# Kernel tuning notes

Measured on AMD Instinct MI355X. Metric: run time of the kernel, lower is better.

## Reference

```python
import jax, jax.numpy as jnp
import numpy as np

B, F, D, H = 16384, 39, 16, 2   # batch, fields, embed_dim, heads
VOCAB = 10000                    # per-field vocab
DH = D * H                       # attention output dim per layer (no head split)


def setup_inputs() -> dict:
    key = jax.random.key(0)
    ks = jax.random.split(key, 32)
    def n(k, shape, s=0.05):
        return jax.random.normal(k, shape, jnp.float32) * s
    inp = {"x": jax.random.randint(ks[0], (B, F), 0, VOCAB, dtype=jnp.int32)}
    inp["emb"] = n(ks[1], (F * VOCAB, D))
    idx = 2
    for i, din in enumerate([D, DH, DH]):  # layer0: 16->32, layers 1-2: 32->32
        for nm in ["wq", "wk", "wv", "wr"]:
            inp[f"{nm}{i}"] = n(ks[idx], (din, DH)); idx += 1
    prev = F * DH  # 1248 after flatten
    for i, u in enumerate([128, 64, 32, 1], 1):
        inp[f"w{i}"] = n(ks[idx], (prev, u)); idx += 1
        inp[f"b{i}"] = jnp.zeros((u,), jnp.float32)
        prev = u
    return inp


def reference(x, emb,
              wq0, wk0, wv0, wr0,
              wq1, wk1, wv1, wr1,
              wq2, wk2, wv2, wr2,
              w1, b1, w2, b2, w3, b3, w4, b4):
    offsets = jnp.arange(F, dtype=jnp.int32) * VOCAB
    e = emb[x + offsets]                                   # [B, F, D]
    for wq, wk, wv, wr in [(wq0, wk0, wv0, wr0),
                           (wq1, wk1, wv1, wr1),
                           (wq2, wk2, wv2, wr2)]:
        q = jnp.einsum('bfd,de->bfe', e, wq)               # [B, F, DH]
        k = jnp.einsum('bfd,de->bfe', e, wk)
        v = jnp.einsum('bfd,de->bfe', e, wv)
        att = jax.nn.softmax(jnp.einsum('bfe,bge->bfg', q, k), axis=-1)  # [B,F,F], no scaling
        out = jnp.einsum('bfg,bge->bfe', att, v) + jnp.einsum('bfd,de->bfe', e, wr)
        e = jax.nn.relu(out)
    h = e.reshape(B, F * DH)
    for w, b in [(w1, b1), (w2, b2), (w3, b3)]:
        h = jax.nn.relu(h @ w + b)
    return jax.nn.sigmoid(h @ w4 + b4)                     # [B, 1]
```

## Files before the change

### kernel.cpp

```cpp
#include <hip/hip_runtime.h>
#include <math.h>

#define NF   39
#define NB   16384
#define NVOC 10000

typedef unsigned short u16;
typedef unsigned int   u32;
typedef float f32x4 __attribute__((ext_vector_type(4)));
typedef float f32x2 __attribute__((ext_vector_type(2)));
typedef short s16x8 __attribute__((ext_vector_type(8)));
typedef unsigned int u32x2 __attribute__((ext_vector_type(2)));

#define E3_U16   20447232u
#define WOFF_W1  9216u
#define NSWZ     179200

__device__ __forceinline__ u32 bfadj(float x){
    u32 u = __float_as_uint(x);
    return u + 0x7fffu + ((u >> 16) & 1u);
}
__device__ __forceinline__ u32 pk2(float a, float b){
#if __has_builtin(__builtin_amdgcn_cvt_pk_bf16_f32)
    auto t = __builtin_amdgcn_cvt_pk_bf16_f32(a, b);
    u32 r; __builtin_memcpy(&r, &t, 4); return r;
#else
    return __builtin_amdgcn_perm(bfadj(a), bfadj(b), 0x03020706u);
#endif
}
__device__ __forceinline__ u16 f2bf(float f){ return (u16)(bfadj(f) >> 16); }

__device__ __forceinline__ float fexp2(float x){
#if __has_builtin(__builtin_amdgcn_exp2f)
    return __builtin_amdgcn_exp2f(x);
#else
    return exp2f(x);
#endif
}
__device__ __forceinline__ float frcp(float x){
#if __has_builtin(__builtin_amdgcn_rcpf)
    return __builtin_amdgcn_rcpf(x);
#else
    return 1.f / x;
#endif
}

__device__ __forceinline__ void wave_sync(){
    asm volatile("s_waitcnt lgkmcnt(0)" ::: "memory");
}
__device__ __forceinline__ f32x4 mfma16(s16x8 a, s16x8 b, f32x4 c){
    return __builtin_amdgcn_mfma_f32_16x16x32_bf16(a, b, c, 0, 0, 0);
}
__device__ __forceinline__ void store4(u16* p, f32x4 v){
    *(uint2*)p = make_uint2(pk2(v[0], v[1]), pk2(v[2], v[3]));
}

__device__ __forceinline__ f32x2 pkadd(f32x2 a, f32x2 b){
    f32x2 d; asm("v_pk_add_f32 %0, %1, %2" : "=v"(d) : "v"(a), "v"(b)); return d;
}
__device__ __forceinline__ f32x2 pkmul(f32x2 a, f32x2 b){
    f32x2 d; asm("v_pk_mul_f32 %0, %1, %2" : "=v"(d) : "v"(a), "v"(b)); return d;
}

__device__ __forceinline__ void swap32(u32 &a, u32 &b){
    asm("v_permlane32_swap_b32 %0, %1" : "+v"(a), "+v"(b));
}
__device__ __forceinline__ void swap16(u32 &a, u32 &b){
    asm("v_permlane16_swap_b32 %0, %1" : "+v"(a), "+v"(b));
}
__device__ __forceinline__ s16x8 fragPack(u32 a0, u32 a1, u32 b0, u32 b1){
    swap32(a0, b0); swap16(a0, b0);
    swap32(a1, b1); swap16(a1, b1);
    union { u32 w[4]; s16x8 v; } u;
    u.w[0] = a0; u.w[1] = a1; u.w[2] = b0; u.w[3] = b1;
    return u.v;
}
__device__ __forceinline__ s16x8 fragCC(f32x4 A, f32x4 B){
    return fragPack(pk2(A[0],A[1]), pk2(A[2],A[3]), pk2(B[0],B[1]), pk2(B[2],B[3]));
}
__device__ __forceinline__ s16x8 fragC0(f32x4 A){
    return fragPack(pk2(A[0],A[1]), pk2(A[2],A[3]), 0u, 0u);
}
__device__ __forceinline__ s16x8 fragCCn(f32x4 A, f32x4 B, f32x2 iv){
    f32x2 a01 = pkmul(__builtin_shufflevector(A, A, 0, 1), iv);
    f32x2 a23 = pkmul(__builtin_shufflevector(A, A, 2, 3), iv);
    f32x2 b01 = pkmul(__builtin_shufflevector(B, B, 0, 1), iv);
    f32x2 b23 = pkmul(__builtin_shufflevector(B, B, 2, 3), iv);
    return fragPack(pk2(a01.x,a01.y), pk2(a23.x,a23.y),
                    pk2(b01.x,b01.y), pk2(b23.x,b23.y));
}
__device__ __forceinline__ s16x8 fragC0n(f32x4 A, f32x2 iv){
    f32x2 a01 = pkmul(__builtin_shufflevector(A, A, 0, 1), iv);
    f32x2 a23 = pkmul(__builtin_shufflevector(A, A, 2, 3), iv);
    return fragPack(pk2(a01.x,a01.y), pk2(a23.x,a23.y), 0u, 0u);
}
__device__ __forceinline__ float xadd16(float t){
    u32 a = __float_as_uint(t), b = a;
    swap16(a, b);
    return __uint_as_float(a) + __uint_as_float(b);
}
__device__ __forceinline__ float xadd32(float t){
    u32 a = __float_as_uint(t), b = a;
    swap32(a, b);
    return __uint_as_float(a) + __uint_as_float(b);
}

__global__ void __launch_bounds__(256) swz_kernel(
    const float* __restrict__ wq0, const float* __restrict__ wk0,
    const float* __restrict__ wv0, const float* __restrict__ wr0,
    const float* __restrict__ wq1, const float* __restrict__ wk1,
    const float* __restrict__ wv1, const float* __restrict__ wr1,
    const float* __restrict__ wq2, const float* __restrict__ wk2,
    const float* __restrict__ wv2, const float* __restrict__ wr2,
    const float* __restrict__ w1, const float* __restrict__ w2,
    const float* __restrict__ w3, u16* __restrict__ ws)
{
    int gid = (int)blockIdx.x*256 + (int)threadIdx.x;
    if (gid >= NSWZ) return;
    int w    = gid & 511;
    int lane = w >> 3, j = w & 7;
    int n    = lane & 15, quad = lane >> 4;
    int kin  = quad*8 + j;
    float val;
    if (gid < 9216){
        int l = gid / 3072;
        int rr = gid - l*3072;
        int kind = rr >> 10;
        int a    = (rr >> 9) & 1;
        int din  = l ? 32 : 16;
        const float *WQ, *WK, *WV, *WR;
        if (l == 0){ WQ=wq0; WK=wk0; WV=wv0; WR=wr0; }
        else if (l == 1){ WQ=wq1; WK=wk1; WV=wv1; WR=wr1; }
        else { WQ=wq2; WK=wk2; WV=wv2; WR=wr2; }
        if (kind == 0){
            int dp = a*16 + n;
            float s = 0.f;
            if (dp < din && kin < din){
                float acc = 0.f;
                for (int e = 0; e < 32; ++e)
                    acc += WQ[kin*32 + e] * WK[dp*32 + e];
                s = acc * 1.44269504f;
            }
            val = s;
        } else {
            const float* W = (kind == 1) ? WV : WR;
            val = (kin < din) ? W[kin*32 + a*16 + n] : 0.f;
        }
    } else if (gid < 9216 + 159744){
        int tt = (gid - 9216) >> 9;
        int ks = tt >> 3, nt = tt & 7;
        val = w1[(ks*32 + kin)*128 + nt*16 + n];
    } else if (gid < 9216 + 159744 + 8192){
        int tt = (gid - (9216+159744)) >> 9;
        int ks = tt >> 2, nt = tt & 3;
        val = w2[(ks*32 + kin)*64 + nt*16 + n];
    } else {
        int tt = (gid - (9216+159744+8192)) >> 9;
        int ks = tt >> 1, nt = tt & 1;
        val = w3[(ks*32 + kin)*32 + nt*16 + n];
    }
    ws[E3_U16 + gid] = f2bf(val);
}

__global__ void __launch_bounds__(256, 4) attn_kernel(
    const int* __restrict__ x, const float* __restrict__ emb,
    u16* __restrict__ ws)
{
    __shared__ __align__(16) u16 lds[4*1536];
    const int tid  = (int)threadIdx.x;
    const int wid  = tid >> 6, lane = tid & 63;
    const int h    = lane >> 4, nl = lane & 15;
    const int r    = (int)blockIdx.x*4 + wid;

    u16* eBuf = lds + wid*1536;
    const u16* wmat = ws + E3_U16;
    const f32x4 z = {0.f, 0.f, 0.f, 0.f};

    f32x4 ci;
#pragma unroll
    for (int reg = 0; reg < 4; ++reg)
        ci[reg] = (h*4 + reg >= 7) ? -1e30f : 0.f;

    if (lane < 48){
        int f = lane, mt = f >> 4, fl = f & 15;
        u16* row = eBuf + mt*512 + fl*8;
        if (f < NF){
            const float4* ep = (const float4*)(emb + ((size_t)(x[r*NF + f] + f*NVOC))*16);
            float4 e0 = ep[0], e1 = ep[1], e2 = ep[2], e3 = ep[3];
            *(uint4*)(row)       = make_uint4(pk2(e0.x,e0.y), pk2(e0.z,e0.w),
                                              pk2(e1.x,e1.y), pk2(e1.z,e1.w));
            *(uint4*)(row + 128) = make_uint4(pk2(e2.x,e2.y), pk2(e2.z,e2.w),
                                              pk2(e3.x,e3.y), pk2(e3.z,e3.w));
        } else {
            *(uint4*)(row)       = make_uint4(0,0,0,0);
            *(uint4*)(row + 128) = make_uint4(0,0,0,0);
        }
        *(uint4*)(row + 256) = make_uint4(0,0,0,0);
        *(uint4*)(row + 384) = make_uint4(0,0,0,0);
    }
    wave_sync();
    s16x8 bE[3];
#pragma unroll
    for (int nt = 0; nt < 3; ++nt)
        bE[nt] = *(const s16x8*)(eBuf + nt*512 + lane*8);

#pragma unroll 1
    for (int L = 0; L < 3; ++L){
        const u16* wL = wmat + L*3072;

        s16x8 bT[3];
        {
            s16x8 g0 = *(const s16x8*)(wL +       lane*8);
            s16x8 g1 = *(const s16x8*)(wL + 512 + lane*8);
#pragma unroll
            for (int nt = 0; nt < 3; ++nt)
                bT[nt] = fragCC(mfma16(g0, bE[nt], z), mfma16(g1, bE[nt], z));
        }
        s16x8 aV[2][2];
        {
            s16x8 v0 = *(const s16x8*)(wL + 1024 + lane*8);
            s16x8 v1 = *(const s16x8*)(wL + 1536 + lane*8);
#pragma unroll
            for (int emt = 0; emt < 2; ++emt){
                s16x8 vb = emt ? v1 : v0;
                f32x4 c0 = mfma16(bE[0], vb, z);
                f32x4 c1 = mfma16(bE[1], vb, z);
                f32x4 c2 = mfma16(bE[2], vb, z);
                aV[0][emt] = fragCC(c0, c1);
                aV[1][emt] = fragC0(c2);
            }
        }
        f32x4 S[3][3];
#pragma unroll
        for (int mtg = 0; mtg < 3; ++mtg)
#pragma unroll
        for (int nt = 0; nt < 3; ++nt)
            S[mtg][nt] = mfma16(bE[mtg], bT[nt], (mtg == 2) ? ci : z);

        float inv[3];
#pragma unroll
        for (int nt = 0; nt < 3; ++nt){
            f32x2 acc2 = {0.f, 0.f};
#pragma unroll
            for (int mtg = 0; mtg < 3; ++mtg){
#pragma unroll
                for (int reg = 0; reg < 4; ++reg)
                    S[mtg][nt][reg] = fexp2(S[mtg][nt][reg]);
                acc2 = pkadd(acc2, __builtin_shufflevector(S[mtg][nt], S[mtg][nt], 0, 1));
                acc2 = pkadd(acc2, __builtin_shufflevector(S[mtg][nt], S[mtg][nt], 2, 3));
            }
            inv[nt] = frcp(xadd32(xadd16(acc2.x + acc2.y)));
        }
        inv[2] = (nl < 7) ? inv[2] : 0.f;

        f32x4 R[2][3];
        {
            s16x8 r0 = *(const s16x8*)(wL + 2048 + lane*8);
            s16x8 r1 = *(const s16x8*)(wL + 2560 + lane*8);
#pragma unroll
            for (int nt = 0; nt < 3; ++nt){
                R[0][nt] = mfma16(r0, bE[nt], z);
                R[1][nt] = mfma16(r1, bE[nt], z);
            }
        }
        if (nl >= 7){ R[0][2] = z; R[1][2] = z; }

        if (L < 2){
#pragma unroll
            for (int nt = 0; nt < 3; ++nt){
                f32x2 iv = {inv[nt], inv[nt]};
                s16x8 p0 = fragCCn(S[0][nt], S[1][nt], iv);
                s16x8 p1 = fragC0n(S[2][nt], iv);
                f32x4 oc[2];
#pragma unroll
                for (int emt = 0; emt < 2; ++emt){
                    f32x4 o = mfma16(aV[1][emt], p1,
                              mfma16(aV[0][emt], p0, R[emt][nt]));
#pragma unroll
                    for (int reg = 0; reg < 4; ++reg)
                        o[reg] = fmaxf(o[reg], 0.f);
                    oc[emt] = o;
                }
                bE[nt] = fragCC(oc[0], oc[1]);
            }
        } else {
            int st = r >> 4, sm = r & 15;
            u32 base = (u32)(st*39)*512u + (u32)(sm*8 + (h>>1)*128 + (h&1)*4);
#pragma unroll
            for (int nt = 0; nt < 3; ++nt){
                f32x2 iv = {inv[nt], inv[nt]};
                s16x8 p0 = fragCCn(S[0][nt], S[1][nt], iv);
                s16x8 p1 = fragC0n(S[2][nt], iv);
                int f = nt*16 + nl;
#pragma unroll
                for (int emt = 0; emt < 2; ++emt){
                    f32x4 o = mfma16(aV[1][emt], p1,
                              mfma16(aV[0][emt], p0, R[emt][nt]));
#pragma unroll
                    for (int reg = 0; reg < 4; ++reg)
                        o[reg] = fmaxf(o[reg], 0.f);
                    if (f < NF){
                        u32x2 pkd = { pk2(o[0], o[1]), pk2(o[2], o[3]) };
                        __builtin_nontemporal_store(
                            pkd, (u32x2*)(ws + base + (u32)f*512u + emt*256));
                    }
                }
            }
        }
    }
}

__global__ void __launch_bounds__(256, 4) mlp_kernel(
    const float* __restrict__ b1, const float* __restrict__ b2,
    const float* __restrict__ b3, const float* __restrict__ w4,
    const float* __restrict__ b4, const u16* __restrict__ ws,
    float* __restrict__ out)
{
    __shared__ __align__(16) float red[8192];
    __shared__ __align__(16) u16 h1t[2048];
    __shared__ __align__(16) u16 h2t[1024];
    __shared__ float part[32];
    const int tid = (int)threadIdx.x;
    const int w   = tid >> 6, lane = tid & 63;
    const int h   = lane >> 4, nl = lane & 15;
    const int st  = (int)blockIdx.x;
    const int A_off = nl*8 + (h>>1)*128 + (h&1)*4;

    const u16* w1b = ws + E3_U16 + WOFF_W1;
    const u16* w2b = w1b + 159744u;
    const u16* w3b = w2b + 8192u;
    const f32x4 z = {0.f,0.f,0.f,0.f};

    f32x4 acc[8];
#pragma unroll
    for (int nt = 0; nt < 8; ++nt) acc[nt] = z;
#pragma unroll 2
    for (int ks = w; ks < 39; ks += 4){
        s16x8 aE = __builtin_nontemporal_load(
            (const s16x8*)(ws + (u32)(st*39 + ks)*512u + lane*8));
#pragma unroll
        for (int nt = 0; nt < 8; ++nt){
            s16x8 aW = *(const s16x8*)(w1b + (ks*8 + nt)*512 + lane*8);
            acc[nt] = mfma16(aW, aE, acc[nt]);
        }
    }
#pragma unroll
    for (int nt = 0; nt < 8; ++nt)
        *(f32x4*)(red + (w*8 + nt)*256 + lane*4) = acc[nt];
    __syncthreads();

#pragma unroll
    for (int t = 0; t < 2; ++t){
        int ft = 2*w + t;
        f32x4 s = *(const f32x4*)(red + (0*8 + ft)*256 + lane*4);
#pragma unroll
        for (int p = 1; p < 4; ++p){
            f32x4 q = *(const f32x4*)(red + (p*8 + ft)*256 + lane*4);
#pragma unroll
            for (int reg = 0; reg < 4; ++reg) s[reg] += q[reg];
        }
        float4 bv = *(const float4*)(b1 + ft*16 + h*4);
        f32x4 v;
        v[0] = fmaxf(s[0] + bv.x, 0.f);
        v[1] = fmaxf(s[1] + bv.y, 0.f);
        v[2] = fmaxf(s[2] + bv.z, 0.f);
        v[3] = fmaxf(s[3] + bv.w, 0.f);
        store4(h1t + ft*256 + A_off, v);
    }
    __syncthreads();

    {
        f32x4 a2 = z;
#pragma unroll
        for (int ks = 0; ks < 4; ++ks){
            s16x8 aW = *(const s16x8*)(w2b + (ks*4 + w)*512 + lane*8);
            s16x8 bH = *(const s16x8*)(h1t + ks*512 + lane*8);
            a2 = mfma16(aW, bH, a2);
        }
        float4 bv = *(const float4*)(b2 + w*16 + h*4);
        f32x4 v;
        v[0] = fmaxf(a2[0] + bv.x, 0.f);
        v[1] = fmaxf(a2[1] + bv.y, 0.f);
        v[2] = fmaxf(a2[2] + bv.z, 0.f);
        v[3] = fmaxf(a2[3] + bv.w, 0.f);
        store4(h2t + (w>>1)*512 + (w&1)*256 + A_off, v);
    }
    __syncthreads();

    if (w < 2){
        f32x4 a3 = z;
#pragma unroll
        for (int ks = 0; ks < 2; ++ks){
            s16x8 aW = *(const s16x8*)(w3b + (ks*2 + w)*512 + lane*8);
            s16x8 bH = *(const s16x8*)(h2t + ks*512 + lane*8);
            a3 = mfma16(aW, bH, a3);
        }
        float4 b3v = *(const float4*)(b3 + w*16 + h*4);
        float4 w4v = *(const float4*)(w4 + w*16 + h*4);
        float t = fmaxf(a3[0] + b3v.x, 0.f)*w4v.x
                + fmaxf(a3[1] + b3v.y, 0.f)*w4v.y
                + fmaxf(a3[2] + b3v.z, 0.f)*w4v.z
                + fmaxf(a3[3] + b3v.w, 0.f)*w4v.w;
        t += __shfl_xor(t, 16, 64);
        t += __shfl_xor(t, 32, 64);
        if (h == 0) part[w*16 + nl] = t;
    }
    __syncthreads();
    if (tid < 16){
        float zz = part[tid] + part[16 + tid] + b4[0];
        out[st*16 + tid] = 1.f/(1.f + __expf(-zz));
    }
}

extern "C" void kernel_launch(void* const* d_in, const int* in_sizes, int n_in,
                              void* d_out, int out_size, void* d_ws, size_t ws_size,
                              hipStream_t stream)
{
    (void)in_sizes; (void)n_in; (void)ws_size; (void)out_size;
    const int*   x   = (const int*)d_in[0];
    const float* emb = (const float*)d_in[1];
    u16* ws = (u16*)d_ws;

    swz_kernel<<<(NSWZ+255)/256, 256, 0, stream>>>(
        (const float*)d_in[2],  (const float*)d_in[3],  (const float*)d_in[4],  (const float*)d_in[5],
        (const float*)d_in[6],  (const float*)d_in[7],  (const float*)d_in[8],  (const float*)d_in[9],
        (const float*)d_in[10], (const float*)d_in[11], (const float*)d_in[12], (const float*)d_in[13],
        (const float*)d_in[14], (const float*)d_in[16], (const float*)d_in[18], ws);

    attn_kernel<<<NB/4, 256, 0, stream>>>(x, emb, ws);

    mlp_kernel<<<NB/16, 256, 0, stream>>>(
        (const float*)d_in[15], (const float*)d_in[17], (const float*)d_in[19],
        (const float*)d_in[20], (const float*)d_in[21], ws, (float*)d_out);
}
```

Baseline: 196.5 us.

## Give each wave its own MLP row tile and use cached attention stores

The MLP kernel is reorganised so each wave owns a full 16-row tile and runs all 39 K-steps of layer 1, plus layers 2-4, alone. This removes the 32 KB shared-memory reduction buffer and the block-wide barriers, using only wave-level syncs. The grid shrinks to a quarter, with four tiles per block. Separately, the attention kernel's output stores switch from nontemporal to ordinary stores, so the data the MLP kernel reads next may stay in cache. The cost is a longer serial K loop per wave and less latency hiding inside each tile.

```diff
diff --git a/kernel.cpp b/kernel.cpp
--- a/kernel.cpp
+++ b/kernel.cpp
@@ -299,11 +299,9 @@
 #pragma unroll
                     for (int reg = 0; reg < 4; ++reg)
                         o[reg] = fmaxf(o[reg], 0.f);
-                    if (f < NF){
-                        u32x2 pkd = { pk2(o[0], o[1]), pk2(o[2], o[3]) };
-                        __builtin_nontemporal_store(
-                            pkd, (u32x2*)(ws + base + (u32)f*512u + emt*256));
-                    }
+                    if (f < NF)
+                        *(uint2*)(ws + base + (u32)f*512u + emt*256) =
+                            make_uint2(pk2(o[0], o[1]), pk2(o[2], o[3]));
                 }
             }
         }
@@ -316,16 +314,16 @@
     const float* __restrict__ b4, const u16* __restrict__ ws,
     float* __restrict__ out)
 {
-    __shared__ __align__(16) float red[8192];
-    __shared__ __align__(16) u16 h1t[2048];
-    __shared__ __align__(16) u16 h2t[1024];
-    __shared__ float part[32];
+    __shared__ __align__(16) u16 h1t[4*2048];
+    __shared__ __align__(16) u16 h2t[4*1024];
     const int tid = (int)threadIdx.x;
     const int w   = tid >> 6, lane = tid & 63;
     const int h   = lane >> 4, nl = lane & 15;
-    const int st  = (int)blockIdx.x;
+    const int st  = (int)blockIdx.x*4 + w;
     const int A_off = nl*8 + (h>>1)*128 + (h&1)*4;
 
+    u16* h1w = h1t + w*2048;
+    u16* h2w = h2t + w*1024;
     const u16* w1b = ws + E3_U16 + WOFF_W1;
     const u16* w2b = w1b + 159744u;
     const u16* w3b = w2b + 8192u;
@@ -335,7 +333,7 @@
 #pragma unroll
     for (int nt = 0; nt < 8; ++nt) acc[nt] = z;
 #pragma unroll 2
-    for (int ks = w; ks < 39; ks += 4){
+    for (int ks = 0; ks < 39; ++ks){
         s16x8 aE = __builtin_nontemporal_load(
             (const s16x8*)(ws + (u32)(st*39 + ks)*512u + lane*8));
 #pragma unroll
@@ -345,70 +343,67 @@
         }
     }
 #pragma unroll
-    for (int nt = 0; nt < 8; ++nt)
-        *(f32x4*)(red + (w*8 + nt)*256 + lane*4) = acc[nt];
-    __syncthreads();
-
-#pragma unroll
-    for (int t = 0; t < 2; ++t){
-        int ft = 2*w + t;
-        f32x4 s = *(const f32x4*)(red + (0*8 + ft)*256 + lane*4);
-#pragma unroll
-        for (int p = 1; p < 4; ++p){
-            f32x4 q = *(const f32x4*)(red + (p*8 + ft)*256 + lane*4);
-#pragma unroll
-            for (int reg = 0; reg < 4; ++reg) s[reg] += q[reg];
-        }
-        float4 bv = *(const float4*)(b1 + ft*16 + h*4);
+    for (int nt = 0; nt < 8; ++nt){
+        float4 bv = *(const float4*)(b1 + nt*16 + h*4);
         f32x4 v;
-        v[0] = fmaxf(s[0] + bv.x, 0.f);
-        v[1] = fmaxf(s[1] + bv.y, 0.f);
-        v[2] = fmaxf(s[2] + bv.z, 0.f);
-        v[3] = fmaxf(s[3] + bv.w, 0.f);
-        store4(h1t + ft*256 + A_off, v);
-    }
-    __syncthreads();
+        v[0] = fmaxf(acc[nt][0] + bv.x, 0.f);
+        v[1] = fmaxf(acc[nt][1] + bv.y, 0.f);
+        v[2] = fmaxf(acc[nt][2] + bv.z, 0.f);
+        v[3] = fmaxf(acc[nt][3] + bv.w, 0.f);
+        store4(h1w + nt*256 + A_off, v);
+    }
+    wave_sync();
 
     {
-        f32x4 a2 = z;
+        f32x4 a2[4];
+#pragma unroll
+        for (int nt = 0; nt < 4; ++nt) a2[nt] = z;
 #pragma unroll
         for (int ks = 0; ks < 4; ++ks){
-            s16x8 aW = *(const s16x8*)(w2b + (ks*4 + w)*512 + lane*8);
-            s16x8 bH = *(const s16x8*)(h1t + ks*512 + lane*8);
-            a2 = mfma16(aW, bH, a2);
-        }
-        float4 bv = *(const float4*)(b2 + w*16 + h*4);
-        f32x4 v;
-        v[0] = fmaxf(a2[0] + bv.x, 0.f);
-        v[1] = fmaxf(a2[1] + bv.y, 0.f);
-        v[2] = fmaxf(a2[2] + bv.z, 0.f);
-        v[3] = fmaxf(a2[3] + bv.w, 0.f);
-        store4(h2t + (w>>1)*512 + (w&1)*256 + A_off, v);
-    }
-    __syncthreads();
-
-    if (w < 2){
-        f32x4 a3 = z;
-#pragma unroll
-        for (int ks = 0; ks < 2; ++ks){
-            s16x8 aW = *(const s16x8*)(w3b + (ks*2 + w)*512 + lane*8);
-            s16x8 bH = *(const s16x8*)(h2t + ks*512 + lane*8);
-            a3 = mfma16(aW, bH, a3);
-        }
-        float4 b3v = *(const float4*)(b3 + w*16 + h*4);
-        float4 w4v = *(const float4*)(w4 + w*16 + h*4);
-        float t = fmaxf(a3[0] + b3v.x, 0.f)*w4v.x
-                + fmaxf(a3[1] + b3v.y, 0.f)*w4v.y
-                + fmaxf(a3[2] + b3v.z, 0.f)*w4v.z
-                + fmaxf(a3[3] + b3v.w, 0.f)*w4v.w;
+            s16x8 bH = *(const s16x8*)(h1w + ks*512 + lane*8);
+#pragma unroll
+            for (int nt = 0; nt < 4; ++nt){
+                s16x8 aW = *(const s16x8*)(w2b + (ks*4 + nt)*512 + lane*8);
+                a2[nt] = mfma16(aW, bH, a2[nt]);
+            }
+        }
+#pragma unroll
+        for (int nt = 0; nt < 4; ++nt){
+            float4 bv = *(const float4*)(b2 + nt*16 + h*4);
+            f32x4 v;
+            v[0] = fmaxf(a2[nt][0] + bv.x, 0.f);
+            v[1] = fmaxf(a2[nt][1] + bv.y, 0.f);
+            v[2] = fmaxf(a2[nt][2] + bv.z, 0.f);
+            v[3] = fmaxf(a2[nt][3] + bv.w, 0.f);
+            store4(h2w + (nt>>1)*512 + (nt&1)*256 + A_off, v);
+        }
+    }
+    wave_sync();
+
+    {
+        float t = 0.f;
+#pragma unroll
+        for (int nt = 0; nt < 2; ++nt){
+            f32x4 a3 = z;
+#pragma unroll
+            for (int ks = 0; ks < 2; ++ks){
+                s16x8 aW = *(const s16x8*)(w3b + (ks*2 + nt)*512 + lane*8);
+                s16x8 bH = *(const s16x8*)(h2w + ks*512 + lane*8);
+                a3 = mfma16(aW, bH, a3);
+            }
+            float4 b3v = *(const float4*)(b3 + nt*16 + h*4);
+            float4 w4v = *(const float4*)(w4 + nt*16 + h*4);
+            t += fmaxf(a3[0] + b3v.x, 0.f)*w4v.x
+               + fmaxf(a3[1] + b3v.y, 0.f)*w4v.y
+               + fmaxf(a3[2] + b3v.z, 0.f)*w4v.z
+               + fmaxf(a3[3] + b3v.w, 0.f)*w4v.w;
+        }
         t += __shfl_xor(t, 16, 64);
         t += __shfl_xor(t, 32, 64);
-        if (h == 0) part[w*16 + nl] = t;
-    }
-    __syncthreads();
-    if (tid < 16){
-        float zz = part[tid] + part[16 + tid] + b4[0];
-        out[st*16 + tid] = 1.f/(1.f + __expf(-zz));
+        if (h == 0){
+            float zz = t + b4[0];
+            out[st*16 + nl] = 1.f/(1.f + __expf(-zz));
+        }
     }
 }
 
@@ -429,7 +424,7 @@
 
     attn_kernel<<<NB/4, 256, 0, stream>>>(x, emb, ws);
 
-    mlp_kernel<<<NB/16, 256, 0, stream>>>(
+    mlp_kernel<<<NB/64, 256, 0, stream>>>(
         (const float*)d_in[15], (const float*)d_in[17], (const float*)d_in[19],
         (const float*)d_in[20], (const float*)d_in[21], ws, (float*)d_out);
 }
```

Result: slower. 203.4 us (+3.5%).
